# Kernel tuning notes

Hardware: AMD Instinct MI355X
Metric: run time of the kernel (lower is better)

Reference implementation:

```python
import jax, jax.numpy as jnp
import numpy as np

BOS = 1  # TOKENS['BOS'] assumed


def gru_scan(x_seq, h0, W_ih, W_hh, b_ih, b_hh):
    """PyTorch-style single-layer GRU over time. x_seq: (T,B,H), h0: (B,H)."""
    def step(h, x):
        gi = x @ W_ih.T + b_ih          # (B,3H)
        gh = h @ W_hh.T + b_hh          # (B,3H)
        i_r, i_z, i_n = jnp.split(gi, 3, axis=-1)
        h_r, h_z, h_n = jnp.split(gh, 3, axis=-1)
        r = jax.nn.sigmoid(i_r + h_r)
        z = jax.nn.sigmoid(i_z + h_z)
        n = jnp.tanh(i_n + r * h_n)
        h_new = (1.0 - z) * n + z * h
        return h_new, h_new
    hT, outs = jax.lax.scan(step, h0, x_seq)
    return outs, hT


def setup_inputs() -> dict:
    key = jax.random.key(0)
    ks = jax.random.split(key, 24)
    H = 256
    V = 50003       # user_size + 3
    TAGV = 966
    T_in, T_tgt, T_tag, B = 50, 40, 20, 32
    s = 0.02
    inp = {
        'input_tensor': jax.random.randint(ks[0], (T_in, B), 0, V),
        'target_tensor': jax.random.randint(ks[1], (T_tgt, B), 0, V),
        'tag_tensor': jax.random.randint(ks[2], (T_tag, B), 0, TAGV),
        'enc_emb': jax.random.normal(ks[3], (V, H), jnp.float32) * s,
        'enc_Wih': jax.random.normal(ks[4], (3 * H, H), jnp.float32) * s,
        'enc_Whh': jax.random.normal(ks[5], (3 * H, H), jnp.float32) * s,
        'enc_bih': jax.random.normal(ks[6], (3 * H,), jnp.float32) * s,
        'enc_bhh': jax.random.normal(ks[7], (3 * H,), jnp.float32) * s,
        'tag_emb': jax.random.normal(ks[8], (TAGV, H), jnp.float32) * s,
        'tag_Wih': jax.random.normal(ks[9], (3 * H, H), jnp.float32) * s,
        'tag_Whh': jax.random.normal(ks[10], (3 * H, H), jnp.float32) * s,
        'tag_bih': jax.random.normal(ks[11], (3 * H,), jnp.float32) * s,
        'tag_bhh': jax.random.normal(ks[12], (3 * H,), jnp.float32) * s,
        'proj_W': jax.random.normal(ks[13], (H, 2 * H), jnp.float32) * s,
        'proj_b': jax.random.normal(ks[14], (H,), jnp.float32) * s,
        'dec_Wih': jax.random.normal(ks[15], (3 * H, H), jnp.float32) * s,
        'dec_Whh': jax.random.normal(ks[16], (3 * H, H), jnp.float32) * s,
        'dec_bih': jax.random.normal(ks[17], (3 * H,), jnp.float32) * s,
        'dec_bhh': jax.random.normal(ks[18], (3 * H,), jnp.float32) * s,
        'out_W': jax.random.normal(ks[19], (V, H), jnp.float32) * s,
        'out_b': jax.random.normal(ks[20], (V,), jnp.float32) * s,
    }
    return inp


def reference(input_tensor, target_tensor, tag_tensor,
              enc_emb, enc_Wih, enc_Whh, enc_bih, enc_bhh,
              tag_emb, tag_Wih, tag_Whh, tag_bih, tag_bhh,
              proj_W, proj_b,
              dec_Wih, dec_Whh, dec_bih, dec_bhh,
              out_W, out_b):
    T_in, B = input_tensor.shape
    T_tgt = target_tensor.shape[0]
    H = enc_emb.shape[1]
    h0 = jnp.zeros((B, H), enc_emb.dtype)

    # encoder over input tokens
    _, enc_h = gru_scan(enc_emb[input_tensor], h0, enc_Wih, enc_Whh, enc_bih, enc_bhh)
    # tag encoder
    _, tag_h = gru_scan(tag_emb[tag_tensor], h0, tag_Wih, tag_Whh, tag_bih, tag_bhh)

    # proj(cat(tag_hidden, encoder_hidden)); dropout = identity (eval)
    merged = jnp.concatenate([tag_h, enc_h], axis=-1) @ proj_W.T + proj_b  # (B,H)

    # teacher forcing: decoder inputs = [BOS, target[:-1]]
    dec_in = jnp.concatenate(
        [jnp.full((1, B), BOS, dtype=target_tensor.dtype), target_tensor[:-1]], axis=0)
    dec_x = jax.nn.relu(enc_emb[dec_in])                 # (T_tgt,B,H), shared embedding
    dec_outs, _ = gru_scan(dec_x, merged, dec_Wih, dec_Whh, dec_bih, dec_bhh)
    logits = dec_outs @ out_W.T + out_b                  # (T_tgt,B,V)

    # criterion = CrossEntropyLoss(mean over batch), summed over timesteps
    logp = jax.nn.log_softmax(logits, axis=-1)
    nll = -jnp.take_along_axis(logp, target_tensor[..., None], axis=-1)[..., 0]  # (T_tgt,B)
    decoder_loss = nll.mean(axis=1).sum()
    avg_loss = decoder_loss / T_tgt
    decoder_outputs = logits[:, None, :, :]              # (T_tgt,1,B,V) like torch.stack of unsqueezed
    return (decoder_loss, avg_loss, decoder_outputs)
```

## Files before the change

kernel.cpp:

```cpp
#include <hip/hip_runtime.h>
#include <hip/hip_bf16.h>
#include <math.h>


#define H 256
#define H3 768
#define NBATCH 32
#define TIN 50
#define TTGT 40
#define TTAG 20
#define VSZ 50003
#define VP 50048
#define NT 782
#define MT 1280
#define NGI 330
#define NCVT 12512

typedef float f32x4 __attribute__((ext_vector_type(4)));
typedef short short8 __attribute__((ext_vector_type(8)));

__device__ __forceinline__ float dot4(float4 a, float4 b) {
    return a.x * b.x + a.y * b.y + a.z * b.z + a.w * b.w;
}

__device__ __forceinline__ float bf2f(short s) {
    unsigned int u = ((unsigned int)(unsigned short)s) << 16;
    return __builtin_bit_cast(float, u);
}

__device__ __forceinline__ void bar_lgkm() {
    asm volatile("s_waitcnt lgkmcnt(0)" ::: "memory");
    __builtin_amdgcn_s_barrier();
    __builtin_amdgcn_sched_barrier(0);
}

__global__ void k_prep(const float* eWih, const float* tWih, const float* dWih,
                       const float* projW, const float* eWhh, const float* tWhh,
                       const float* dWhh, float* d0, float* d1, float* d2,
                       float* d3, __hip_bfloat16* p0, __hip_bfloat16* p1,
                       __hip_bfloat16* p2) {
    int which = blockIdx.y;
    if (which < 4) {
        const float* s;
        float* d;
        int N, K;
        switch (which) {
            case 0: s = eWih; d = d0; N = H3; K = H; break;
            case 1: s = tWih; d = d1; N = H3; K = H; break;
            case 2: s = dWih; d = d2; N = H3; K = H; break;
            default: s = projW; d = d3; N = H; K = 2 * H; break;
        }
        int n = blockIdx.x;
        if (n >= N) return;
        for (int k = threadIdx.x; k < K; k += 256)
            d[(size_t)(k >> 2) * (N * 4) + n * 4 + (k & 3)] = s[(size_t)n * K + k];
    } else {
        if (blockIdx.x >= 96) return;
        const float* s = which == 4 ? eWhh : (which == 5 ? tWhh : dWhh);
        __hip_bfloat16* d = which == 4 ? p0 : (which == 5 ? p1 : p2);
        int idx = blockIdx.x * 256 + threadIdx.x;
        int lane = idx & 63;
        int f = (idx >> 6) % 24;
        int w = idx / (24 * 64);
        int ks = f / 3, q = f % 3;
        int row = (q << 8) + (w << 4) + (lane & 15);
        int k = (ks << 5) + ((lane >> 4) << 3);
#pragma unroll
        for (int j = 0; j < 8; ++j)
            d[(size_t)idx * 8 + j] = __float2bfloat16(s[(size_t)row * H + k + j]);
    }
}

__global__ __launch_bounds__(256) void k_gi_cvt(
    const int* in_toks, const int* tag_toks, const int* tgt_toks,
    const float* enc_emb, const float* tag_emb, const float* W4e,
    const float* W4t, const float* W4d, const float* bih_e, const float* bhh_e,
    const float* bih_t, const float* bhh_t, const float* bih_d,
    const float* bhh_d, __hip_bfloat16* gi_e, __hip_bfloat16* gi_t,
    __hip_bfloat16* gi_d, const float* outW, __hip_bfloat16* outWb) {
    int bx = blockIdx.x, tid = threadIdx.x;
    if (bx >= NGI) {
        int i4 = ((bx - NGI) * 256 + tid) * 4;
        if (i4 >= VP * H) return;
        int row = i4 >> 8;
        float4 v;
        if (row < VSZ) v = *(const float4*)(outW + i4);
        else v = make_float4(0.f, 0.f, 0.f, 0.f);
        outWb[i4 + 0] = __float2bfloat16(v.x);
        outWb[i4 + 1] = __float2bfloat16(v.y);
        outWb[i4 + 2] = __float2bfloat16(v.z);
        outWb[i4 + 3] = __float2bfloat16(v.w);
        return;
    }
    __shared__ float x[NBATCH][H];
    int g = bx % 3, tt = bx / 3;
    const int* toks;
    const float* emb;
    const float* W4;
    const float* bihp;
    const float* bhhp;
    __hip_bfloat16* gip;
    int t, mode;
    if (tt < TIN) {
        toks = in_toks; emb = enc_emb; W4 = W4e; bihp = bih_e; bhhp = bhh_e;
        gip = gi_e; t = tt; mode = 0;
    } else if (tt < TIN + TTAG) {
        toks = tag_toks; emb = tag_emb; W4 = W4t; bihp = bih_t; bhhp = bhh_t;
        gip = gi_t; t = tt - TIN; mode = 0;
    } else {
        toks = tgt_toks; emb = enc_emb; W4 = W4d; bihp = bih_d; bhhp = bhh_d;
        gip = gi_d; t = tt - TIN - TTAG; mode = 2;
    }
#pragma unroll 4
    for (int b = 0; b < NBATCH; ++b) {
        int tok;
        if (mode == 2) tok = (t == 0) ? 1 : toks[(t - 1) * NBATCH + b];
        else tok = toks[t * NBATCH + b];
        float v = emb[(size_t)tok * H + tid];
        if (mode == 2) v = fmaxf(v, 0.0f);
        x[b][tid] = v;
    }
    __syncthreads();
    int nb_ = tid & 63, mg = tid >> 6;
    float acc[4][8];
#pragma unroll
    for (int j = 0; j < 4; ++j)
#pragma unroll
        for (int mi = 0; mi < 8; ++mi) acc[j][mi] = 0.f;
    for (int k4 = 0; k4 < 64; ++k4) {
        const float4* wrow = (const float4*)(W4 + (size_t)k4 * 3072);
        float4 w0 = wrow[g * 256 + nb_];
        float4 w1 = wrow[g * 256 + nb_ + 64];
        float4 w2 = wrow[g * 256 + nb_ + 128];
        float4 w3 = wrow[g * 256 + nb_ + 192];
#pragma unroll
        for (int mi = 0; mi < 8; ++mi) {
            float4 xv = *(const float4*)&x[mg * 8 + mi][k4 * 4];
            acc[0][mi] += dot4(xv, w0);
            acc[1][mi] += dot4(xv, w1);
            acc[2][mi] += dot4(xv, w2);
            acc[3][mi] += dot4(xv, w3);
        }
    }
#pragma unroll
    for (int j = 0; j < 4; ++j) {
        int n = g * 256 + nb_ + j * 64;
        float bv = bihp[n] + (g < 2 ? bhhp[n] : 0.0f);
        int nn = n & 255;
        int ww = nn >> 4, lrr = nn & 15;
#pragma unroll
        for (int mi = 0; mi < 8; ++mi) {
            int bm = mg * 8 + mi;
            int locb = bm >> 4, lmm = bm & 15;
            int lgg = lmm >> 2, reg = lmm & 3;
            size_t idx = ((size_t)(t * 2 + locb) * 16 + ww) * 1024 +
                         reg * 256 + (lgg * 16 + lrr) * 4 + g;
            gip[idx] = __float2bfloat16(acc[j][mi] + bv);
        }
    }
}

__global__ __launch_bounds__(1024) void k_scan(
    int nset1,
    const __hip_bfloat16* gi1, const __hip_bfloat16* W1, const float* bhh1,
    const float* h01, float* hT1, __hip_bfloat16* out1, int T1,
    const __hip_bfloat16* gi2, const __hip_bfloat16* W2, const float* bhh2,
    const float* h02, float* hT2, __hip_bfloat16* out2, int T2) {
    __shared__ uint4 WL[16 * 6 * 64];
    __shared__ uint4 HBF[2][512];

    int blk = blockIdx.x, tid = threadIdx.x;
    const __hip_bfloat16 *gip, *Wg;
    const float *bhh, *h0;
    float* hTp;
    __hip_bfloat16* outp;
    int T, loc;
    if (blk < nset1) {
        gip = gi1; Wg = W1; bhh = bhh1; h0 = h01; hTp = hT1; outp = out1;
        T = T1; loc = blk;
    } else {
        gip = gi2; Wg = W2; bhh = bhh2; h0 = h02; hTp = hT2; outp = out2;
        T = T2; loc = blk - nset1;
    }
    int mb = loc * 16;
    int w = tid >> 6, lane = tid & 63, lr = lane & 15, lg = lane >> 4;

    short8 wreg[18];
    const uint4* Wg4 = (const uint4*)Wg;
#pragma unroll
    for (int f = 0; f < 18; ++f) {
        uint4 v = Wg4[(size_t)(w * 24 + f) * 64 + lane];
        wreg[f] = *(short8*)&v;
    }
#pragma unroll
    for (int i = 0; i < 6; ++i)
        WL[(w * 6 + i) * 64 + lane] = Wg4[(size_t)(w * 24 + 18 + i) * 64 + lane];

    float bnv = bhh[512 + w * 16 + lr];

    float hprev[4];
    short* HB16 = (short*)HBF;
#pragma unroll
    for (int reg = 0; reg < 4; ++reg) {
        int row = lg * 4 + reg, col = w * 16 + lr;
        float hv = h0 ? h0[(size_t)(mb + row) * H + col] : 0.0f;
        hprev[reg] = hv;
        __hip_bfloat16 q = __float2bfloat16(hv);
        int ch = w * 2 + (lr >> 3);
        int slot = ch ^ (row & 7);
        HB16[row * 256 + slot * 8 + (lr & 7)] = *(short*)&q;
    }
    uint2 gv[4];
    {
        const __hip_bfloat16* gp = gip + ((size_t)loc * 16 + w) * 1024;
#pragma unroll
        for (int reg = 0; reg < 4; ++reg)
            gv[reg] = *(const uint2*)(gp + reg * 256 + lane * 4);
    }
    __syncthreads();

    const short8* HSbase = (const short8*)HBF;
    const short8* WLs = (const short8*)WL;
    for (int t = 0; t < T; ++t) {
        int p = t & 1, p2 = p ^ 1;
        const short8* HS = HSbase + p * 512;
        f32x4 acc[3];
        acc[0] = (f32x4){0.f, 0.f, 0.f, 0.f};
        acc[1] = acc[0];
        acc[2] = (f32x4){bnv, bnv, bnv, bnv};
#pragma unroll
        for (int ks = 0; ks < 6; ++ks) {
            short8 a = HS[lr * 32 + ((ks * 4 + lg) ^ (lr & 7))];
#pragma unroll
            for (int q = 0; q < 3; ++q)
                acc[q] = __builtin_amdgcn_mfma_f32_16x16x32_bf16(
                    a, wreg[ks * 3 + q], acc[q], 0, 0, 0);
        }
#pragma unroll
        for (int ks = 6; ks < 8; ++ks) {
            short8 a = HS[lr * 32 + ((ks * 4 + lg) ^ (lr & 7))];
#pragma unroll
            for (int q = 0; q < 3; ++q) {
                short8 bv = WLs[(w * 6 + (ks - 6) * 3 + q) * 64 + lane];
                acc[q] = __builtin_amdgcn_mfma_f32_16x16x32_bf16(
                    a, bv, acc[q], 0, 0, 0);
            }
        }
#pragma unroll
        for (int reg = 0; reg < 4; ++reg) {
            uint2 u = gv[reg];
            float gr = bf2f((short)(u.x & 0xffff));
            float gz = bf2f((short)(u.x >> 16));
            float gn = bf2f((short)(u.y & 0xffff));
            float er = __expf(-(gr + acc[0][reg]));
            float r = __builtin_amdgcn_rcpf(1.0f + er);
            float ez = __expf(-(gz + acc[1][reg]));
            float z = __builtin_amdgcn_rcpf(1.0f + ez);
            float xx = gn + r * acc[2][reg];
            float e2 = __expf(-2.0f * fabsf(xx));
            float nv = copysignf((1.0f - e2) * __builtin_amdgcn_rcpf(1.0f + e2), xx);
            float hnew = (1.0f - z) * nv + z * hprev[reg];
            hprev[reg] = hnew;
            __hip_bfloat16 qb = __float2bfloat16(hnew);
            int row = lg * 4 + reg;
            int ch = w * 2 + (lr >> 3);
            int slot = ch ^ (row & 7);
            HB16[p2 * 4096 + row * 256 + slot * 8 + (lr & 7)] = *(short*)&qb;
        }
        if (t + 1 < T) {
            const __hip_bfloat16* gp =
                gip + ((size_t)((t + 1) * 2 + loc) * 16 + w) * 1024;
#pragma unroll
            for (int reg = 0; reg < 4; ++reg)
                gv[reg] = *(const uint2*)(gp + reg * 256 + lane * 4);
        }
        if (outp && t >= 1 && tid < 512) {
            int lb = tid >> 5, ch2 = tid & 31;
            short8 hv = HSbase[p * 512 + lb * 32 + (ch2 ^ (lb & 7))];
            *(short8*)(outp + (size_t)((t - 1) * NBATCH + mb + lb) * H + ch2 * 8) = hv;
        }
        bar_lgkm();
    }
    if (outp && tid < 512) {
        int lb = tid >> 5, ch2 = tid & 31;
        short8 hv = HSbase[(T & 1) * 512 + lb * 32 + (ch2 ^ (lb & 7))];
        *(short8*)(outp + (size_t)((T - 1) * NBATCH + mb + lb) * H + ch2 * 8) = hv;
    }
    if (hTp) {
#pragma unroll
        for (int reg = 0; reg < 4; ++reg) {
            int row = lg * 4 + reg, col = w * 16 + lr;
            hTp[(size_t)(mb + row) * H + col] = hprev[reg];
        }
    }
}

__global__ void k_proj(const float* tag_h, const float* enc_h,
                       const float* W4p, const float* pb, float* merged) {
    __shared__ float c[2 * H];
    int b = blockIdx.x, tid = threadIdx.x;
    c[tid] = tag_h[b * H + tid];
    c[H + tid] = enc_h[b * H + tid];
    __syncthreads();
    float acc = 0.f;
#pragma unroll 4
    for (int k4 = 0; k4 < 128; ++k4) {
        float4 cv = *(const float4*)&c[k4 * 4];
        float4 wv = ((const float4*)(W4p + (size_t)k4 * 1024))[tid];
        acc += dot4(cv, wv);
    }
    merged[b * H + tid] = acc + pb[tid];
}

__global__ __launch_bounds__(256) void k_logits(const __hip_bfloat16* A,
                                                const __hip_bfloat16* Bw,
                                                const float* bias, float* dout,
                                                float* pmax, float* psum) {
    __shared__ uint4 bsm[2048];
    __shared__ float cst[4][16][68];
    int bid = blockIdx.x;
    int wg = (bid & 7) * 1955 + (bid >> 3);
    int nblk = wg / 20, mblk = wg % 20;
    int m0 = mblk * 64, n0 = nblk * 64;
    int tid = threadIdx.x;
    int wave = tid >> 6, lane = tid & 63, lr = lane & 15, lg = lane >> 4;
    const uint4* Bg = (const uint4*)(Bw + (size_t)n0 * H);
#pragma unroll
    for (int i = 0; i < 8; ++i) {
        int c = tid + i * 256;
        int r = c >> 5, g = c & 31;
        bsm[(r << 5) | (g ^ (r & 7))] = Bg[c];
    }
    short8 areg[8];
    const uint4* Ar = (const uint4*)(A + (size_t)(m0 + wave * 16 + lr) * H);
#pragma unroll
    for (int ks = 0; ks < 8; ++ks) {
        uint4 v = Ar[ks * 4 + lg];
        areg[ks] = *(short8*)&v;
    }
    float biasv[4];
    bool valid[4];
#pragma unroll
    for (int ns = 0; ns < 4; ++ns) {
        int n = n0 + ns * 16 + lr;
        valid[ns] = (n < VSZ);
        biasv[ns] = valid[ns] ? bias[n] : 0.f;
    }
    __syncthreads();
    f32x4 acc[4];
#pragma unroll
    for (int ns = 0; ns < 4; ++ns) acc[ns] = (f32x4){0.f, 0.f, 0.f, 0.f};
    const short8* L = (const short8*)bsm;
#pragma unroll
    for (int ks = 0; ks < 8; ++ks) {
        int ga = ks * 4 + lg;
#pragma unroll
        for (int ns = 0; ns < 4; ++ns) {
            int rb = ns * 16 + lr;
            acc[ns] = __builtin_amdgcn_mfma_f32_16x16x32_bf16(
                areg[ks], L[(rb << 5) | (ga ^ (rb & 7))], acc[ns], 0, 0, 0);
        }
    }
    float* cw = &cst[wave][0][0];
#pragma unroll
    for (int reg = 0; reg < 4; ++reg) {
        int m = m0 + wave * 16 + lg * 4 + reg;
        float v[4];
        float rm = -INFINITY;
#pragma unroll
        for (int ns = 0; ns < 4; ++ns) {
            v[ns] = acc[ns][reg] + biasv[ns];
            if (valid[ns]) rm = fmaxf(rm, v[ns]);
            cw[(lg * 4 + reg) * 68 + ns * 16 + lr] = v[ns];
        }
        for (int off = 1; off < 16; off <<= 1) rm = fmaxf(rm, __shfl_xor(rm, off));
        float se = 0.f;
#pragma unroll
        for (int ns = 0; ns < 4; ++ns)
            if (valid[ns]) se += __expf(v[ns] - rm);
        for (int off = 1; off < 16; off <<= 1) se += __shfl_xor(se, off);
        if (lr == 0) {
            pmax[(size_t)m * NT + nblk] = rm;
            psum[(size_t)m * NT + nblk] = se;
        }
    }
    float* dbase = dout + 2 + (size_t)(m0 + wave * 16) * VSZ + n0;
    int c0 = lr * 4;
    bool full = (n0 + c0 + 3 < VSZ);
#pragma unroll
    for (int it = 0; it < 4; ++it) {
        int row = it * 4 + lg;
        f32x4 v4 = *(const f32x4*)&cst[wave][row][c0];
        float* p = dbase + (size_t)row * VSZ + c0;
        if (full) {
            __builtin_memcpy(p, &v4, 16);
        } else {
#pragma unroll
            for (int j = 0; j < 4; ++j)
                if (n0 + c0 + j < VSZ) p[j] = v4[j];
        }
    }
}

__global__ void k_lse(const float* pmax, const float* psum, float* lse) {
    int m = blockIdx.x, tid = threadIdx.x;
    __shared__ float sm[4];
    float lm = -INFINITY;
    for (int i = tid; i < NT; i += 256) lm = fmaxf(lm, pmax[(size_t)m * NT + i]);
    for (int off = 1; off < 64; off <<= 1) lm = fmaxf(lm, __shfl_xor(lm, off));
    if ((tid & 63) == 0) sm[tid >> 6] = lm;
    __syncthreads();
    float M = fmaxf(fmaxf(sm[0], sm[1]), fmaxf(sm[2], sm[3]));
    __syncthreads();
    float s = 0.f;
    for (int i = tid; i < NT; i += 256)
        s += psum[(size_t)m * NT + i] * __expf(pmax[(size_t)m * NT + i] - M);
    for (int off = 1; off < 64; off <<= 1) s += __shfl_xor(s, off);
    if ((tid & 63) == 0) sm[tid >> 6] = s;
    __syncthreads();
    if (tid == 0) lse[m] = M + logf(sm[0] + sm[1] + sm[2] + sm[3]);
}

__global__ void k_loss(const float* lse, const int* tgt, float* dout) {
    int tid = threadIdx.x;
    __shared__ float sm[4];
    float s = 0.f;
    for (int m = tid; m < MT; m += 256) {
        int tg = tgt[m];
        s += lse[m] - dout[2 + (size_t)m * VSZ + tg];
    }
    for (int off = 1; off < 64; off <<= 1) s += __shfl_xor(s, off);
    if ((tid & 63) == 0) sm[tid >> 6] = s;
    __syncthreads();
    if (tid == 0) {
        float total = sm[0] + sm[1] + sm[2] + sm[3];
        dout[0] = total / 32.0f;
        dout[1] = total / 1280.0f;
    }
}

extern "C" void kernel_launch(void* const* d_in, const int* in_sizes, int n_in,
                              void* d_out, int out_size, void* d_ws,
                              size_t ws_size, hipStream_t stream) {
    const int* input_tensor = (const int*)d_in[0];
    const int* target_tensor = (const int*)d_in[1];
    const int* tag_tensor = (const int*)d_in[2];
    const float* enc_emb = (const float*)d_in[3];
    const float* enc_Wih = (const float*)d_in[4];
    const float* enc_Whh = (const float*)d_in[5];
    const float* enc_bih = (const float*)d_in[6];
    const float* enc_bhh = (const float*)d_in[7];
    const float* tag_emb = (const float*)d_in[8];
    const float* tag_Wih = (const float*)d_in[9];
    const float* tag_Whh = (const float*)d_in[10];
    const float* tag_bih = (const float*)d_in[11];
    const float* tag_bhh = (const float*)d_in[12];
    const float* proj_W = (const float*)d_in[13];
    const float* proj_b = (const float*)d_in[14];
    const float* dec_Wih = (const float*)d_in[15];
    const float* dec_Whh = (const float*)d_in[16];
    const float* dec_bih = (const float*)d_in[17];
    const float* dec_bhh = (const float*)d_in[18];
    const float* out_W = (const float*)d_in[19];
    const float* out_b = (const float*)d_in[20];

    char* wsb = (char*)d_ws;
    size_t o = 0;
    auto alloc = [&](size_t bytes) {
        size_t r = o;
        o += (bytes + 511) & ~(size_t)511;
        return r;
    };
    float* W4_enc_ih = (float*)(wsb + alloc(H3 * H * 4));
    float* W4_tag_ih = (float*)(wsb + alloc(H3 * H * 4));
    float* W4_dec_ih = (float*)(wsb + alloc(H3 * H * 4));
    float* W4_proj   = (float*)(wsb + alloc(H * 2 * H * 4));
    __hip_bfloat16* gi_enc = (__hip_bfloat16*)(wsb + alloc((size_t)TIN * 65536));
    __hip_bfloat16* gi_tag = (__hip_bfloat16*)(wsb + alloc((size_t)TTAG * 65536));
    __hip_bfloat16* gi_dec = (__hip_bfloat16*)(wsb + alloc((size_t)TTGT * 65536));
    float* enc_h  = (float*)(wsb + alloc(NBATCH * H * 4));
    float* tag_h  = (float*)(wsb + alloc(NBATCH * H * 4));
    float* merged = (float*)(wsb + alloc(NBATCH * H * 4));
    float* lse    = (float*)(wsb + alloc(MT * 4));
    __hip_bfloat16* Wp_enc = (__hip_bfloat16*)(wsb + alloc(H3 * H * 2));
    __hip_bfloat16* Wp_tag = (__hip_bfloat16*)(wsb + alloc(H3 * H * 2));
    __hip_bfloat16* Wp_dec = (__hip_bfloat16*)(wsb + alloc(H3 * H * 2));
    __hip_bfloat16* outWb  = (__hip_bfloat16*)(wsb + alloc((size_t)VP * H * 2));
    __hip_bfloat16* decA   = (__hip_bfloat16*)(wsb + alloc((size_t)MT * H * 2));
    float* pmax = (float*)(wsb + alloc((size_t)MT * NT * 4));
    float* psum = (float*)(wsb + alloc((size_t)MT * NT * 4));

    float* dout = (float*)d_out;

    k_prep<<<dim3(H3, 7), 256, 0, stream>>>(
        enc_Wih, tag_Wih, dec_Wih, proj_W, enc_Whh, tag_Whh, dec_Whh,
        W4_enc_ih, W4_tag_ih, W4_dec_ih, W4_proj, Wp_enc, Wp_tag, Wp_dec);

    k_gi_cvt<<<NGI + NCVT, 256, 0, stream>>>(
        input_tensor, tag_tensor, target_tensor, enc_emb, tag_emb, W4_enc_ih,
        W4_tag_ih, W4_dec_ih, enc_bih, enc_bhh, tag_bih, tag_bhh, dec_bih,
        dec_bhh, gi_enc, gi_tag, gi_dec, out_W, outWb);

    k_scan<<<4, 1024, 0, stream>>>(
        2, gi_enc, Wp_enc, enc_bhh, nullptr, enc_h, nullptr, TIN,
        gi_tag, Wp_tag, tag_bhh, nullptr, tag_h, nullptr, TTAG);

    k_proj<<<NBATCH, 256, 0, stream>>>(tag_h, enc_h, W4_proj, proj_b, merged);

    k_scan<<<2, 1024, 0, stream>>>(
        2, gi_dec, Wp_dec, dec_bhh, merged, nullptr, decA, TTGT,
        nullptr, nullptr, nullptr, nullptr, nullptr, nullptr, 0);

    k_logits<<<NT * 20, 256, 0, stream>>>(decA, outWb, out_b, dout, pmax, psum);

    k_lse<<<MT, 256, 0, stream>>>(pmax, psum, lse);

    k_loss<<<1, 256, 0, stream>>>(lse, target_tensor, dout);
}
```

Baseline: 450.8 us.

## Overlap encoder scans with decoder input GEMM and vocab weight conversion

Moves the decoder input-gate GEMM and the large output-weight bf16 conversion into extra blocks of the encoder scan launch, so that work runs on otherwise idle CUs while the 4 latency-bound scan blocks execute. The separate projection kernel is folded into the start of the decoder scan, and the Whh packing and projection-weight transpose move into the gi prep kernel. This cuts the number of launches and takes the bulk conversion off the critical path. The cost is that extra blocks may compete with the scan blocks for memory bandwidth, and each decoder block now recomputes the projection for its own rows.

After: 424.0 us (median of 2 runs). 5.9% less time.

```diff
diff --git a/kernel.cpp b/kernel.cpp
--- a/kernel.cpp
+++ b/kernel.cpp
@@ -13,8 +13,8 @@
 #define VP 50048
 #define NT 782
 #define MT 1280
-#define NGI 330
-#define NCVT 12512
+#define NGIET 210
+#define NCVT2 504
 
 typedef float f32x4 __attribute__((ext_vector_type(4)));
 typedef short short8 __attribute__((ext_vector_type(8)));
@@ -35,30 +35,37 @@
 }
 
 __global__ void k_prep(const float* eWih, const float* tWih, const float* dWih,
-                       const float* projW, const float* eWhh, const float* tWhh,
-                       const float* dWhh, float* d0, float* d1, float* d2,
-                       float* d3, __hip_bfloat16* p0, __hip_bfloat16* p1,
-                       __hip_bfloat16* p2) {
+                       float* d0, float* d1, float* d2) {
     int which = blockIdx.y;
-    if (which < 4) {
-        const float* s;
-        float* d;
-        int N, K;
-        switch (which) {
-            case 0: s = eWih; d = d0; N = H3; K = H; break;
-            case 1: s = tWih; d = d1; N = H3; K = H; break;
-            case 2: s = dWih; d = d2; N = H3; K = H; break;
-            default: s = projW; d = d3; N = H; K = 2 * H; break;
-        }
-        int n = blockIdx.x;
-        if (n >= N) return;
-        for (int k = threadIdx.x; k < K; k += 256)
-            d[(size_t)(k >> 2) * (N * 4) + n * 4 + (k & 3)] = s[(size_t)n * K + k];
-    } else {
-        if (blockIdx.x >= 96) return;
-        const float* s = which == 4 ? eWhh : (which == 5 ? tWhh : dWhh);
-        __hip_bfloat16* d = which == 4 ? p0 : (which == 5 ? p1 : p2);
-        int idx = blockIdx.x * 256 + threadIdx.x;
+    const float* s = which == 0 ? eWih : (which == 1 ? tWih : dWih);
+    float* d = which == 0 ? d0 : (which == 1 ? d1 : d2);
+    int n = blockIdx.x;
+    for (int k = threadIdx.x; k < H; k += 256)
+        d[(size_t)(k >> 2) * (H3 * 4) + n * 4 + (k & 3)] = s[(size_t)n * H + k];
+}
+
+__global__ __launch_bounds__(256) void k_gi_prep(
+    const int* in_toks, const int* tag_toks, const float* enc_emb,
+    const float* tag_emb, const float* W4e, const float* W4t,
+    const float* bih_e, const float* bhh_e, const float* bih_t,
+    const float* bhh_t, __hip_bfloat16* gi_e, __hip_bfloat16* gi_t,
+    const float* eWhh, const float* tWhh, const float* dWhh,
+    __hip_bfloat16* p0, __hip_bfloat16* p1, __hip_bfloat16* p2,
+    const float* projW, float* W4_proj) {
+    int bx = blockIdx.x, tid = threadIdx.x;
+    if (bx >= 498) {
+        int n = bx - 498;
+        for (int k = tid; k < 2 * H; k += 256)
+            W4_proj[(size_t)(k >> 2) * 1024 + n * 4 + (k & 3)] =
+                projW[(size_t)n * 2 * H + k];
+        return;
+    }
+    if (bx >= NGIET) {
+        int wb = bx - NGIET;
+        int m = wb / 96;
+        const float* s = m == 0 ? eWhh : (m == 1 ? tWhh : dWhh);
+        __hip_bfloat16* d = m == 0 ? p0 : (m == 1 ? p1 : p2);
+        int idx = (wb % 96) * 256 + tid;
         int lane = idx & 63;
         int f = (idx >> 6) % 24;
         int w = idx / (24 * 64);
@@ -68,28 +75,6 @@
 #pragma unroll
         for (int j = 0; j < 8; ++j)
             d[(size_t)idx * 8 + j] = __float2bfloat16(s[(size_t)row * H + k + j]);
-    }
-}
-
-__global__ __launch_bounds__(256) void k_gi_cvt(
-    const int* in_toks, const int* tag_toks, const int* tgt_toks,
-    const float* enc_emb, const float* tag_emb, const float* W4e,
-    const float* W4t, const float* W4d, const float* bih_e, const float* bhh_e,
-    const float* bih_t, const float* bhh_t, const float* bih_d,
-    const float* bhh_d, __hip_bfloat16* gi_e, __hip_bfloat16* gi_t,
-    __hip_bfloat16* gi_d, const float* outW, __hip_bfloat16* outWb) {
-    int bx = blockIdx.x, tid = threadIdx.x;
-    if (bx >= NGI) {
-        int i4 = ((bx - NGI) * 256 + tid) * 4;
-        if (i4 >= VP * H) return;
-        int row = i4 >> 8;
-        float4 v;
-        if (row < VSZ) v = *(const float4*)(outW + i4);
-        else v = make_float4(0.f, 0.f, 0.f, 0.f);
-        outWb[i4 + 0] = __float2bfloat16(v.x);
-        outWb[i4 + 1] = __float2bfloat16(v.y);
-        outWb[i4 + 2] = __float2bfloat16(v.z);
-        outWb[i4 + 3] = __float2bfloat16(v.w);
         return;
     }
     __shared__ float x[NBATCH][H];
@@ -100,26 +85,16 @@
     const float* bihp;
     const float* bhhp;
     __hip_bfloat16* gip;
-    int t, mode;
+    int t;
     if (tt < TIN) {
         toks = in_toks; emb = enc_emb; W4 = W4e; bihp = bih_e; bhhp = bhh_e;
-        gip = gi_e; t = tt; mode = 0;
-    } else if (tt < TIN + TTAG) {
+        gip = gi_e; t = tt;
+    } else {
         toks = tag_toks; emb = tag_emb; W4 = W4t; bihp = bih_t; bhhp = bhh_t;
-        gip = gi_t; t = tt - TIN; mode = 0;
-    } else {
-        toks = tgt_toks; emb = enc_emb; W4 = W4d; bihp = bih_d; bhhp = bhh_d;
-        gip = gi_d; t = tt - TIN - TTAG; mode = 2;
-    }
-#pragma unroll 4
-    for (int b = 0; b < NBATCH; ++b) {
-        int tok;
-        if (mode == 2) tok = (t == 0) ? 1 : toks[(t - 1) * NBATCH + b];
-        else tok = toks[t * NBATCH + b];
-        float v = emb[(size_t)tok * H + tid];
-        if (mode == 2) v = fmaxf(v, 0.0f);
-        x[b][tid] = v;
-    }
+        gip = gi_t; t = tt - TIN;
+    }
+    for (int b = 0; b < NBATCH; ++b)
+        x[b][tid] = emb[(size_t)toks[t * NBATCH + b] * H + tid];
     __syncthreads();
     int nb_ = tid & 63, mg = tid >> 6;
     float acc[4][8];
@@ -160,27 +135,96 @@
     }
 }
 
-__global__ __launch_bounds__(1024) void k_scan(
-    int nset1,
+__global__ __launch_bounds__(1024) void k_scan_enc(
     const __hip_bfloat16* gi1, const __hip_bfloat16* W1, const float* bhh1,
-    const float* h01, float* hT1, __hip_bfloat16* out1, int T1,
+    float* hT1, int T1,
     const __hip_bfloat16* gi2, const __hip_bfloat16* W2, const float* bhh2,
-    const float* h02, float* hT2, __hip_bfloat16* out2, int T2) {
+    float* hT2, int T2,
+    const int* tgt_toks, const float* enc_emb, const float* W4d,
+    const float* bih_d, const float* bhh_d, __hip_bfloat16* gi_d,
+    const float* outW, __hip_bfloat16* outWb) {
     __shared__ uint4 WL[16 * 6 * 64];
     __shared__ uint4 HBF[2][512];
 
     int blk = blockIdx.x, tid = threadIdx.x;
+    if (blk >= 4) {
+        int wb = blk - 4;
+        if (wb < TTGT) {
+            int t = wb;
+            float* x = (float*)WL;
+            if (tid < 256) {
+                for (int b = 0; b < NBATCH; ++b) {
+                    int tok = (t == 0) ? 1 : tgt_toks[(t - 1) * NBATCH + b];
+                    x[b * 256 + tid] = fmaxf(enc_emb[(size_t)tok * H + tid], 0.0f);
+                }
+            }
+            __syncthreads();
+            if (tid < 768) {
+                int g = tid >> 8, tidg = tid & 255;
+                int nb_ = tidg & 63, mg = tidg >> 6;
+                float acc[4][8];
+#pragma unroll
+                for (int j = 0; j < 4; ++j)
+#pragma unroll
+                    for (int mi = 0; mi < 8; ++mi) acc[j][mi] = 0.f;
+                for (int k4 = 0; k4 < 64; ++k4) {
+                    const float4* wrow = (const float4*)(W4d + (size_t)k4 * 3072);
+                    float4 w0 = wrow[g * 256 + nb_];
+                    float4 w1 = wrow[g * 256 + nb_ + 64];
+                    float4 w2 = wrow[g * 256 + nb_ + 128];
+                    float4 w3 = wrow[g * 256 + nb_ + 192];
+#pragma unroll
+                    for (int mi = 0; mi < 8; ++mi) {
+                        float4 xv = *(const float4*)&x[(mg * 8 + mi) * 256 + k4 * 4];
+                        acc[0][mi] += dot4(xv, w0);
+                        acc[1][mi] += dot4(xv, w1);
+                        acc[2][mi] += dot4(xv, w2);
+                        acc[3][mi] += dot4(xv, w3);
+                    }
+                }
+#pragma unroll
+                for (int j = 0; j < 4; ++j) {
+                    int n = g * 256 + nb_ + j * 64;
+                    float bv = bih_d[n] + (g < 2 ? bhh_d[n] : 0.0f);
+                    int nn = n & 255;
+                    int ww = nn >> 4, lrr = nn & 15;
+#pragma unroll
+                    for (int mi = 0; mi < 8; ++mi) {
+                        int bm = mg * 8 + mi;
+                        int locb = bm >> 4, lmm = bm & 15;
+                        int lgg = lmm >> 2, reg = lmm & 3;
+                        size_t idx = ((size_t)(t * 2 + locb) * 16 + ww) * 1024 +
+                                     reg * 256 + (lgg * 16 + lrr) * 4 + g;
+                        gi_d[idx] = __float2bfloat16(acc[j][mi] + bv);
+                    }
+                }
+            }
+            return;
+        }
+        const size_t total = (size_t)VP * H / 4;
+        const size_t stride = (size_t)NCVT2 * 1024;
+        for (size_t i = (size_t)(wb - TTGT) * 1024 + tid; i < total; i += stride) {
+            size_t i4 = i * 4;
+            int row = (int)(i4 >> 8);
+            float4 v;
+            if (row < VSZ) v = *(const float4*)(outW + i4);
+            else v = make_float4(0.f, 0.f, 0.f, 0.f);
+            outWb[i4 + 0] = __float2bfloat16(v.x);
+            outWb[i4 + 1] = __float2bfloat16(v.y);
+            outWb[i4 + 2] = __float2bfloat16(v.z);
+            outWb[i4 + 3] = __float2bfloat16(v.w);
+        }
+        return;
+    }
+
     const __hip_bfloat16 *gip, *Wg;
-    const float *bhh, *h0;
+    const float* bhh;
     float* hTp;
-    __hip_bfloat16* outp;
     int T, loc;
-    if (blk < nset1) {
-        gip = gi1; Wg = W1; bhh = bhh1; h0 = h01; hTp = hT1; outp = out1;
-        T = T1; loc = blk;
+    if (blk < 2) {
+        gip = gi1; Wg = W1; bhh = bhh1; hTp = hT1; T = T1; loc = blk;
     } else {
-        gip = gi2; Wg = W2; bhh = bhh2; h0 = h02; hTp = hT2; outp = out2;
-        T = T2; loc = blk - nset1;
+        gip = gi2; Wg = W2; bhh = bhh2; hTp = hT2; T = T2; loc = blk - 2;
     }
     int mb = loc * 16;
     int w = tid >> 6, lane = tid & 63, lr = lane & 15, lg = lane >> 4;
@@ -202,13 +246,11 @@
     short* HB16 = (short*)HBF;
 #pragma unroll
     for (int reg = 0; reg < 4; ++reg) {
-        int row = lg * 4 + reg, col = w * 16 + lr;
-        float hv = h0 ? h0[(size_t)(mb + row) * H + col] : 0.0f;
-        hprev[reg] = hv;
-        __hip_bfloat16 q = __float2bfloat16(hv);
+        int row = lg * 4 + reg;
+        hprev[reg] = 0.0f;
         int ch = w * 2 + (lr >> 3);
         int slot = ch ^ (row & 7);
-        HB16[row * 256 + slot * 8 + (lr & 7)] = *(short*)&q;
+        HB16[row * 256 + slot * 8 + (lr & 7)] = 0;
     }
     uint2 gv[4];
     {
@@ -274,42 +316,165 @@
             for (int reg = 0; reg < 4; ++reg)
                 gv[reg] = *(const uint2*)(gp + reg * 256 + lane * 4);
         }
-        if (outp && t >= 1 && tid < 512) {
+        bar_lgkm();
+    }
+    if (hTp) {
+#pragma unroll
+        for (int reg = 0; reg < 4; ++reg) {
+            int row = lg * 4 + reg, col = w * 16 + lr;
+            hTp[(size_t)(mb + row) * H + col] = hprev[reg];
+        }
+    }
+}
+
+__global__ __launch_bounds__(1024) void k_scan_dec(
+    const __hip_bfloat16* gip, const __hip_bfloat16* Wg, const float* bhh,
+    __hip_bfloat16* outp, int T,
+    const float* tagh, const float* ench, const float* W4p, const float* pb) {
+    __shared__ uint4 WL[16 * 6 * 64];
+    __shared__ uint4 HBF[2][512];
+
+    int blk = blockIdx.x, tid = threadIdx.x;
+    int loc = blk, mb = loc * 16;
+    int w = tid >> 6, lane = tid & 63, lr = lane & 15, lg = lane >> 4;
+
+    float* CC = (float*)WL;
+    float* MM = ((float*)WL) + 8192;
+#pragma unroll
+    for (int i = 0; i < 8; ++i) {
+        int idx = i * 1024 + tid;
+        int row = idx >> 9, col = idx & 511;
+        float v = (col < 256) ? tagh[(size_t)(mb + row) * H + col]
+                              : ench[(size_t)(mb + row) * H + (col - 256)];
+        CC[idx] = v;
+    }
+    __syncthreads();
+    {
+        int col = tid & 255, rg = tid >> 8;
+        float a0 = 0.f, a1 = 0.f, a2 = 0.f, a3 = 0.f;
+        for (int k4 = 0; k4 < 128; ++k4) {
+            float4 wv = ((const float4*)(W4p + (size_t)k4 * 1024))[col];
+            float4 c0 = *(const float4*)&CC[(rg * 4 + 0) * 512 + k4 * 4];
+            float4 c1 = *(const float4*)&CC[(rg * 4 + 1) * 512 + k4 * 4];
+            float4 c2 = *(const float4*)&CC[(rg * 4 + 2) * 512 + k4 * 4];
+            float4 c3 = *(const float4*)&CC[(rg * 4 + 3) * 512 + k4 * 4];
+            a0 += dot4(c0, wv);
+            a1 += dot4(c1, wv);
+            a2 += dot4(c2, wv);
+            a3 += dot4(c3, wv);
+        }
+        float bv = pb[col];
+        __syncthreads();
+        MM[(rg * 4 + 0) * 256 + col] = a0 + bv;
+        MM[(rg * 4 + 1) * 256 + col] = a1 + bv;
+        MM[(rg * 4 + 2) * 256 + col] = a2 + bv;
+        MM[(rg * 4 + 3) * 256 + col] = a3 + bv;
+    }
+    __syncthreads();
+
+    float hprev[4];
+    short* HB16 = (short*)HBF;
+#pragma unroll
+    for (int reg = 0; reg < 4; ++reg) {
+        int row = lg * 4 + reg, col = w * 16 + lr;
+        float hv = MM[row * 256 + col];
+        hprev[reg] = hv;
+        __hip_bfloat16 q = __float2bfloat16(hv);
+        int ch = w * 2 + (lr >> 3);
+        int slot = ch ^ (row & 7);
+        HB16[row * 256 + slot * 8 + (lr & 7)] = *(short*)&q;
+    }
+    __syncthreads();
+
+    short8 wreg[18];
+    const uint4* Wg4 = (const uint4*)Wg;
+#pragma unroll
+    for (int f = 0; f < 18; ++f) {
+        uint4 v = Wg4[(size_t)(w * 24 + f) * 64 + lane];
+        wreg[f] = *(short8*)&v;
+    }
+#pragma unroll
+    for (int i = 0; i < 6; ++i)
+        WL[(w * 6 + i) * 64 + lane] = Wg4[(size_t)(w * 24 + 18 + i) * 64 + lane];
+
+    float bnv = bhh[512 + w * 16 + lr];
+
+    uint2 gv[4];
+    {
+        const __hip_bfloat16* gp = gip + ((size_t)loc * 16 + w) * 1024;
+#pragma unroll
+        for (int reg = 0; reg < 4; ++reg)
+            gv[reg] = *(const uint2*)(gp + reg * 256 + lane * 4);
+    }
+    __syncthreads();
+
+    const short8* HSbase = (const short8*)HBF;
+    const short8* WLs = (const short8*)WL;
+    for (int t = 0; t < T; ++t) {
+        int p = t & 1, p2 = p ^ 1;
+        const short8* HS = HSbase + p * 512;
+        f32x4 acc[3];
+        acc[0] = (f32x4){0.f, 0.f, 0.f, 0.f};
+        acc[1] = acc[0];
+        acc[2] = (f32x4){bnv, bnv, bnv, bnv};
+#pragma unroll
+        for (int ks = 0; ks < 6; ++ks) {
+            short8 a = HS[lr * 32 + ((ks * 4 + lg) ^ (lr & 7))];
+#pragma unroll
+            for (int q = 0; q < 3; ++q)
+                acc[q] = __builtin_amdgcn_mfma_f32_16x16x32_bf16(
+                    a, wreg[ks * 3 + q], acc[q], 0, 0, 0);
+        }
+#pragma unroll
+        for (int ks = 6; ks < 8; ++ks) {
+            short8 a = HS[lr * 32 + ((ks * 4 + lg) ^ (lr & 7))];
+#pragma unroll
+            for (int q = 0; q < 3; ++q) {
+                short8 bv = WLs[(w * 6 + (ks - 6) * 3 + q) * 64 + lane];
+                acc[q] = __builtin_amdgcn_mfma_f32_16x16x32_bf16(
+                    a, bv, acc[q], 0, 0, 0);
+            }
+        }
+#pragma unroll
+        for (int reg = 0; reg < 4; ++reg) {
+            uint2 u = gv[reg];
+            float gr = bf2f((short)(u.x & 0xffff));
+            float gz = bf2f((short)(u.x >> 16));
+            float gn = bf2f((short)(u.y & 0xffff));
+            float er = __expf(-(gr + acc[0][reg]));
+            float r = __builtin_amdgcn_rcpf(1.0f + er);
+            float ez = __expf(-(gz + acc[1][reg]));
+            float z = __builtin_amdgcn_rcpf(1.0f + ez);
+            float xx = gn + r * acc[2][reg];
+            float e2 = __expf(-2.0f * fabsf(xx));
+            float nv = copysignf((1.0f - e2) * __builtin_amdgcn_rcpf(1.0f + e2), xx);
+            float hnew = (1.0f - z) * nv + z * hprev[reg];
+            hprev[reg] = hnew;
+            __hip_bfloat16 qb = __float2bfloat16(hnew);
+            int row = lg * 4 + reg;
+            int ch = w * 2 + (lr >> 3);
+            int slot = ch ^ (row & 7);
+            HB16[p2 * 4096 + row * 256 + slot * 8 + (lr & 7)] = *(short*)&qb;
+        }
+        if (t + 1 < T) {
+            const __hip_bfloat16* gp =
+                gip + ((size_t)((t + 1) * 2 + loc) * 16 + w) * 1024;
+#pragma unroll
+            for (int reg = 0; reg < 4; ++reg)
+                gv[reg] = *(const uint2*)(gp + reg * 256 + lane * 4);
+        }
+        if (t >= 1 && tid < 512) {
             int lb = tid >> 5, ch2 = tid & 31;
             short8 hv = HSbase[p * 512 + lb * 32 + (ch2 ^ (lb & 7))];
             *(short8*)(outp + (size_t)((t - 1) * NBATCH + mb + lb) * H + ch2 * 8) = hv;
         }
         bar_lgkm();
     }
-    if (outp && tid < 512) {
+    if (tid < 512) {
         int lb = tid >> 5, ch2 = tid & 31;
         short8 hv = HSbase[(T & 1) * 512 + lb * 32 + (ch2 ^ (lb & 7))];
         *(short8*)(outp + (size_t)((T - 1) * NBATCH + mb + lb) * H + ch2 * 8) = hv;
     }
-    if (hTp) {
-#pragma unroll
-        for (int reg = 0; reg < 4; ++reg) {
-            int row = lg * 4 + reg, col = w * 16 + lr;
-            hTp[(size_t)(mb + row) * H + col] = hprev[reg];
-        }
-    }
-}
-
-__global__ void k_proj(const float* tag_h, const float* enc_h,
-                       const float* W4p, const float* pb, float* merged) {
-    __shared__ float c[2 * H];
-    int b = blockIdx.x, tid = threadIdx.x;
-    c[tid] = tag_h[b * H + tid];
-    c[H + tid] = enc_h[b * H + tid];
-    __syncthreads();
-    float acc = 0.f;
-#pragma unroll 4
-    for (int k4 = 0; k4 < 128; ++k4) {
-        float4 cv = *(const float4*)&c[k4 * 4];
-        float4 wv = ((const float4*)(W4p + (size_t)k4 * 1024))[tid];
-        acc += dot4(cv, wv);
-    }
-    merged[b * H + tid] = acc + pb[tid];
 }
 
 __global__ __launch_bounds__(256) void k_logits(const __hip_bfloat16* A,
@@ -480,7 +645,6 @@
     __hip_bfloat16* gi_dec = (__hip_bfloat16*)(wsb + alloc((size_t)TTGT * 65536));
     float* enc_h  = (float*)(wsb + alloc(NBATCH * H * 4));
     float* tag_h  = (float*)(wsb + alloc(NBATCH * H * 4));
-    float* merged = (float*)(wsb + alloc(NBATCH * H * 4));
     float* lse    = (float*)(wsb + alloc(MT * 4));
     __hip_bfloat16* Wp_enc = (__hip_bfloat16*)(wsb + alloc(H3 * H * 2));
     __hip_bfloat16* Wp_tag = (__hip_bfloat16*)(wsb + alloc(H3 * H * 2));
@@ -492,24 +656,22 @@
 
     float* dout = (float*)d_out;
 
-    k_prep<<<dim3(H3, 7), 256, 0, stream>>>(
-        enc_Wih, tag_Wih, dec_Wih, proj_W, enc_Whh, tag_Whh, dec_Whh,
-        W4_enc_ih, W4_tag_ih, W4_dec_ih, W4_proj, Wp_enc, Wp_tag, Wp_dec);
-
-    k_gi_cvt<<<NGI + NCVT, 256, 0, stream>>>(
-        input_tensor, tag_tensor, target_tensor, enc_emb, tag_emb, W4_enc_ih,
-        W4_tag_ih, W4_dec_ih, enc_bih, enc_bhh, tag_bih, tag_bhh, dec_bih,
-        dec_bhh, gi_enc, gi_tag, gi_dec, out_W, outWb);
-
-    k_scan<<<4, 1024, 0, stream>>>(
-        2, gi_enc, Wp_enc, enc_bhh, nullptr, enc_h, nullptr, TIN,
-        gi_tag, Wp_tag, tag_bhh, nullptr, tag_h, nullptr, TTAG);
-
-    k_proj<<<NBATCH, 256, 0, stream>>>(tag_h, enc_h, W4_proj, proj_b, merged);
-
-    k_scan<<<2, 1024, 0, stream>>>(
-        2, gi_dec, Wp_dec, dec_bhh, merged, nullptr, decA, TTGT,
-        nullptr, nullptr, nullptr, nullptr, nullptr, nullptr, 0);
+    k_prep<<<dim3(H3, 3), 256, 0, stream>>>(enc_Wih, tag_Wih, dec_Wih,
+                                            W4_enc_ih, W4_tag_ih, W4_dec_ih);
+
+    k_gi_prep<<<754, 256, 0, stream>>>(
+        input_tensor, tag_tensor, enc_emb, tag_emb, W4_enc_ih, W4_tag_ih,
+        enc_bih, enc_bhh, tag_bih, tag_bhh, gi_enc, gi_tag,
+        enc_Whh, tag_Whh, dec_Whh, Wp_enc, Wp_tag, Wp_dec, proj_W, W4_proj);
+
+    k_scan_enc<<<4 + TTGT + NCVT2, 1024, 0, stream>>>(
+        gi_enc, Wp_enc, enc_bhh, enc_h, TIN,
+        gi_tag, Wp_tag, tag_bhh, tag_h, TTAG,
+        target_tensor, enc_emb, W4_dec_ih, dec_bih, dec_bhh, gi_dec,
+        out_W, outWb);
+
+    k_scan_dec<<<2, 1024, 0, stream>>>(gi_dec, Wp_dec, dec_bhh, decA, TTGT,
+                                       tag_h, enc_h, W4_proj, proj_b);
 
     k_logits<<<NT * 20, 256, 0, stream>>>(decA, outWb, out_b, dout, pmax, psum);
 
```
